# Kernel optimization log

Measured on AMD Instinct MI355X. Metric: run time of the kernel, lower is better.

## Reference

```python
import jax, jax.numpy as jnp
import numpy as np
import math

NEG_INF = -1e30  # stand-in for float('-inf'); softmax/logsumexp treat it identically


def _fnoise(x):
    # factorized NoisyNet transform f(x) = sign(x) * sqrt(|x|)
    return jnp.sign(x) * jnp.sqrt(jnp.abs(x))


def setup_inputs() -> dict:
    B, T, D, E = 4, 4096, 2048, 16
    key = jax.random.key(0)
    ks = jax.random.split(key, 6)
    sigma_init = 0.4 / math.sqrt(D)  # sigma_zero / sqrt(in_features)
    return {
        "mh_output": jax.random.normal(ks[0], (B, T, D), dtype=jnp.float32),
        "weight": jax.random.normal(ks[1], (E, D), dtype=jnp.float32) * 0.02,
        "sigma_weight": jnp.full((E, D), sigma_init, dtype=jnp.float32),
        "bias": jax.random.normal(ks[2], (E,), dtype=jnp.float32) * 0.02,
        "sigma_bias": jnp.full((E,), sigma_init, dtype=jnp.float32),
        "eps_in": jax.random.normal(ks[3], (D,), dtype=jnp.float32),
        "eps_out": jax.random.normal(ks[4], (E,), dtype=jnp.float32),
    }


def reference(mh_output, weight, sigma_weight, bias, sigma_bias, eps_in, eps_out):
    top_k = 2
    E = weight.shape[0]

    # NoisyFactorizedLinear: W' = W + sigma_W * (f(eps_out) f(eps_in)^T)
    f_in = _fnoise(eps_in)            # [D]
    f_out = _fnoise(eps_out)          # [E]
    w_noisy = weight + sigma_weight * (f_out[:, None] * f_in[None, :])  # [E, D]
    b_noisy = bias + sigma_bias * f_out                                 # [E]
    logits = jnp.einsum("btd,ed->bte", mh_output, w_noisy) + b_noisy    # [B,T,E]
    # dropout(p=0.125) is identity in eval mode

    top_vals, indices = jax.lax.top_k(logits, top_k)                    # [B,T,k]
    # scatter top-k back into a -inf-filled tensor == mask of selected experts
    keep = jnp.sum(jax.nn.one_hot(indices, E, dtype=jnp.bool_), axis=-2)  # [B,T,E]
    sparse_logits = jnp.where(keep, logits, NEG_INF)

    router_output = jax.nn.softmax(sparse_logits, axis=-1)

    # z-loss: mean(logsumexp(sparse_logits, -1)^2); only top-k entries survive
    lse = jax.scipy.special.logsumexp(top_vals, axis=-1)                # [B,T]
    z_loss = jnp.mean(lse ** 2)

    return router_output, indices, z_loss
```

## Files before the change

kernel.cpp:

```cpp
#include <hip/hip_runtime.h>
#include <math.h>

#define NROWS 16384
#define DDIM  2048
#define NEXP  16
#define RBLOCKS 512
#define WPB 8

__device__ __forceinline__ float fnoise(float x) {
    return copysignf(sqrtf(fabsf(x)), x);
}


__global__ void prep_kernel(const float* __restrict__ weight,
                            const float* __restrict__ sigma_weight,
                            const float* __restrict__ bias,
                            const float* __restrict__ sigma_bias,
                            const float* __restrict__ eps_in,
                            const float* __restrict__ eps_out,
                            float* __restrict__ w_noisy,
                            float* __restrict__ b_noisy) {
    int idx = blockIdx.x * blockDim.x + threadIdx.x;
    int e = idx >> 11;
    int d = idx & (DDIM - 1);
    float fi = fnoise(eps_in[d]);
    float fo = fnoise(eps_out[e]);
    w_noisy[idx] = weight[idx] + sigma_weight[idx] * fo * fi;
    if (idx < NEXP) {
        b_noisy[idx] = bias[idx] + sigma_bias[idx] * fnoise(eps_out[idx]);
    }
}

__global__ __launch_bounds__(512, 4) void router_kernel(
        const float* __restrict__ x,
        const float* __restrict__ w_noisy,
        const float* __restrict__ b_noisy,
        float* __restrict__ out_router,
        float* __restrict__ out_idx,
        float* __restrict__ zpart) {
    __shared__ float4 wlds[NEXP * 256];

    const int tid  = threadIdx.x;
    const int wv   = tid >> 6;
    const int lane = tid & 63;

    const int rowBase = blockIdx.x * 32 + wv * 4;
    const float4* xr0 = (const float4*)(x + (size_t)(rowBase + 0) * DDIM);
    const float4* xr1 = (const float4*)(x + (size_t)(rowBase + 1) * DDIM);
    const float4* xr2 = (const float4*)(x + (size_t)(rowBase + 2) * DDIM);
    const float4* xr3 = (const float4*)(x + (size_t)(rowBase + 3) * DDIM);

    float acc[64];
    #pragma unroll
    for (int i = 0; i < 64; ++i) acc[i] = 0.0f;

    const float4* wsrc = (const float4*)w_noisy;

    for (int c = 0; c < 2; ++c) {
        if (c) __syncthreads();
        #pragma unroll
        for (int j = 0; j < 8; ++j) {
            int f = j * 512 + tid;
            wlds[f] = wsrc[(f >> 8) * 512 + c * 256 + (f & 255)];
        }
        __syncthreads();

        #pragma unroll 2
        for (int k = 0; k < 4; ++k) {
            int p  = c * 256 + k * 64 + lane;
            int dd = k * 64 + lane;
            float4 xv0 = xr0[p];
            float4 xv1 = xr1[p];
            float4 xv2 = xr2[p];
            float4 xv3 = xr3[p];
            #pragma unroll
            for (int e = 0; e < 16; ++e) {
                float4 w = wlds[e * 256 + dd];
                float s0 = acc[0 * 16 + e];
                float s1 = acc[1 * 16 + e];
                float s2 = acc[2 * 16 + e];
                float s3 = acc[3 * 16 + e];
                s0 = fmaf(xv0.x, w.x, s0); s0 = fmaf(xv0.y, w.y, s0);
                s0 = fmaf(xv0.z, w.z, s0); s0 = fmaf(xv0.w, w.w, s0);
                s1 = fmaf(xv1.x, w.x, s1); s1 = fmaf(xv1.y, w.y, s1);
                s1 = fmaf(xv1.z, w.z, s1); s1 = fmaf(xv1.w, w.w, s1);
                s2 = fmaf(xv2.x, w.x, s2); s2 = fmaf(xv2.y, w.y, s2);
                s2 = fmaf(xv2.z, w.z, s2); s2 = fmaf(xv2.w, w.w, s2);
                s3 = fmaf(xv3.x, w.x, s3); s3 = fmaf(xv3.y, w.y, s3);
                s3 = fmaf(xv3.z, w.z, s3); s3 = fmaf(xv3.w, w.w, s3);
                acc[0 * 16 + e] = s0;
                acc[1 * 16 + e] = s1;
                acc[2 * 16 + e] = s2;
                acc[3 * 16 + e] = s3;
            }
        }
    }

    #pragma unroll
    for (int half = 32; half >= 1; half >>= 1) {
        #pragma unroll
        for (int i = 0; i < half; ++i) {
            bool hi = (lane & half) != 0;
            float keep = hi ? acc[i + half] : acc[i];
            float send = hi ? acc[i] : acc[i + half];
            float recv = __shfl_xor(send, half, 64);
            acc[i] = keep + recv;
        }
    }

    const int e = lane & 15;
    const int r = lane >> 4;
    const int row = rowBase + r;
    float logit = acc[0] + b_noisy[e];

    float m1 = logit; int i1 = e;
    #pragma unroll
    for (int off = 8; off >= 1; off >>= 1) {
        float om = __shfl_xor(m1, off, 64);
        int   oi = __shfl_xor(i1, off, 64);
        if (om > m1 || (om == m1 && oi < i1)) { m1 = om; i1 = oi; }
    }
    float v2 = (e == i1) ? -3.4e38f : logit;
    float m2 = v2; int i2 = e;
    #pragma unroll
    for (int off = 8; off >= 1; off >>= 1) {
        float om = __shfl_xor(m2, off, 64);
        int   oi = __shfl_xor(i2, off, 64);
        if (om > m2 || (om == m2 && oi < i2)) { m2 = om; i2 = oi; }
    }

    float t = expf(m2 - m1);
    float p1 = 1.0f / (1.0f + t);
    float val = (e == i1) ? p1 : ((e == i2) ? t * p1 : 0.0f);
    out_router[(size_t)rowBase * NEXP + lane] = val;

    if (e < 2) {
        out_idx[(size_t)row * 2 + e] = (float)((e == 0) ? i1 : i2);
    }

    float zv = 0.0f;
    if (e == 0) {
        float lse = m1 + log1pf(t);
        zv = lse * lse;
    }
    zv += __shfl_xor(zv, 16, 64);
    zv += __shfl_xor(zv, 32, 64);
    if (lane == 0) {
        zpart[blockIdx.x * WPB + wv] = zv;
    }
}

__global__ void finalize_kernel(const float* __restrict__ zpart,
                                float* __restrict__ out) {
    __shared__ float ws4[4];
    int tid = threadIdx.x;
    float s = 0.0f;
    for (int i = tid; i < RBLOCKS * WPB; i += 256) s += zpart[i];
    #pragma unroll
    for (int off = 32; off >= 1; off >>= 1) s += __shfl_xor(s, off, 64);
    if ((tid & 63) == 0) ws4[tid >> 6] = s;
    __syncthreads();
    if (tid == 0) {
        float total = ws4[0] + ws4[1] + ws4[2] + ws4[3];
        out[NROWS * NEXP + NROWS * 2] = total * (1.0f / (float)NROWS);
    }
}

extern "C" void kernel_launch(void* const* d_in, const int* in_sizes, int n_in,
                              void* d_out, int out_size, void* d_ws, size_t ws_size,
                              hipStream_t stream) {
    const float* mh      = (const float*)d_in[0];
    const float* weight  = (const float*)d_in[1];
    const float* sigw    = (const float*)d_in[2];
    const float* bias    = (const float*)d_in[3];
    const float* sigb    = (const float*)d_in[4];
    const float* eps_in  = (const float*)d_in[5];
    const float* eps_out = (const float*)d_in[6];

    float* out      = (float*)d_out;
    float* w_noisy  = (float*)d_ws;
    float* b_noisy  = w_noisy + NEXP * DDIM;
    float* zpart    = w_noisy + 32800;

    prep_kernel<<<(NEXP * DDIM) / 256, 256, 0, stream>>>(
        weight, sigw, bias, sigb, eps_in, eps_out, w_noisy, b_noisy);

    router_kernel<<<RBLOCKS, 512, 0, stream>>>(
        mh, w_noisy, b_noisy, out, out + NROWS * NEXP, zpart);

    finalize_kernel<<<1, 256, 0, stream>>>(zpart, out);
}
```

Baseline: 215.5 us.

## Double-buffer weight chunks in LDS and prefetch x in smaller blocks

The router kernel now uses 256-thread blocks covering 16 rows, with twice as many blocks. It streams the noisy weight matrix through two 16 KB LDS buffers in 64-float4 chunks, and prefetches the next chunk of x rows and weights into registers while the current chunk is computed. This hides global load latency behind the FMAs and should raise occupancy through the smaller LDS footprint. The cost is extra registers for the prefetch buffers and more barriers and total weight reloads across the larger grid.

```diff
diff --git a/kernel.cpp b/kernel.cpp
--- a/kernel.cpp
+++ b/kernel.cpp
@@ -4,8 +4,9 @@
 #define NROWS 16384
 #define DDIM  2048
 #define NEXP  16
-#define RBLOCKS 512
-#define WPB 8
+#define RBLOCKS 1024
+#define WPB 4
+#define ZN (RBLOCKS * WPB)
 
 __device__ __forceinline__ float fnoise(float x) {
     return copysignf(sqrtf(fabsf(x)), x);
@@ -31,70 +32,89 @@
     }
 }
 
-__global__ __launch_bounds__(512, 4) void router_kernel(
+__global__ __launch_bounds__(256, 4) void router_kernel(
         const float* __restrict__ x,
         const float* __restrict__ w_noisy,
         const float* __restrict__ b_noisy,
         float* __restrict__ out_router,
         float* __restrict__ out_idx,
         float* __restrict__ zpart) {
-    __shared__ float4 wlds[NEXP * 256];
+    __shared__ float4 wlds[2][NEXP * 64];
 
     const int tid  = threadIdx.x;
     const int wv   = tid >> 6;
     const int lane = tid & 63;
 
-    const int rowBase = blockIdx.x * 32 + wv * 4;
+    const int rowBase = blockIdx.x * 16 + wv * 4;
     const float4* xr0 = (const float4*)(x + (size_t)(rowBase + 0) * DDIM);
     const float4* xr1 = (const float4*)(x + (size_t)(rowBase + 1) * DDIM);
     const float4* xr2 = (const float4*)(x + (size_t)(rowBase + 2) * DDIM);
     const float4* xr3 = (const float4*)(x + (size_t)(rowBase + 3) * DDIM);
+    const float4* wsrc = (const float4*)w_noisy;
 
     float acc[64];
     #pragma unroll
     for (int i = 0; i < 64; ++i) acc[i] = 0.0f;
 
-    const float4* wsrc = (const float4*)w_noisy;
-
-    for (int c = 0; c < 2; ++c) {
-        if (c) __syncthreads();
+    float4 xA[4], xB[4], wt[4];
+
+    xA[0] = xr0[lane]; xA[1] = xr1[lane]; xA[2] = xr2[lane]; xA[3] = xr3[lane];
+    #pragma unroll
+    for (int j = 0; j < 4; ++j) {
+        int f = j * 256 + tid;
+        wt[j] = wsrc[(f >> 6) * 512 + (f & 63)];
+    }
+    #pragma unroll
+    for (int j = 0; j < 4; ++j) wlds[0][j * 256 + tid] = wt[j];
+    __syncthreads();
+
+    auto chunk_step = [&](int c, float4 (&xc)[4], float4 (&xn)[4],
+                          const float4* __restrict__ wcur,
+                          float4* __restrict__ wnxt) {
+        if (c < 7) {
+            int p = (c + 1) * 64 + lane;
+            xn[0] = xr0[p]; xn[1] = xr1[p]; xn[2] = xr2[p]; xn[3] = xr3[p];
+            #pragma unroll
+            for (int j = 0; j < 4; ++j) {
+                int f = j * 256 + tid;
+                wt[j] = wsrc[(f >> 6) * 512 + (c + 1) * 64 + (f & 63)];
+            }
+        }
         #pragma unroll
-        for (int j = 0; j < 8; ++j) {
-            int f = j * 512 + tid;
-            wlds[f] = wsrc[(f >> 8) * 512 + c * 256 + (f & 255)];
-        }
-        __syncthreads();
-
-        #pragma unroll 2
-        for (int k = 0; k < 4; ++k) {
-            int p  = c * 256 + k * 64 + lane;
-            int dd = k * 64 + lane;
-            float4 xv0 = xr0[p];
-            float4 xv1 = xr1[p];
-            float4 xv2 = xr2[p];
-            float4 xv3 = xr3[p];
+        for (int e = 0; e < 16; ++e) {
+            float4 w = wcur[e * 64 + lane];
+            float s0 = acc[0 * 16 + e];
+            float s1 = acc[1 * 16 + e];
+            float s2 = acc[2 * 16 + e];
+            float s3 = acc[3 * 16 + e];
+            s0 = fmaf(xc[0].x, w.x, s0); s0 = fmaf(xc[0].y, w.y, s0);
+            s0 = fmaf(xc[0].z, w.z, s0); s0 = fmaf(xc[0].w, w.w, s0);
+            s1 = fmaf(xc[1].x, w.x, s1); s1 = fmaf(xc[1].y, w.y, s1);
+            s1 = fmaf(xc[1].z, w.z, s1); s1 = fmaf(xc[1].w, w.w, s1);
+            s2 = fmaf(xc[2].x, w.x, s2); s2 = fmaf(xc[2].y, w.y, s2);
+            s2 = fmaf(xc[2].z, w.z, s2); s2 = fmaf(xc[2].w, w.w, s2);
+            s3 = fmaf(xc[3].x, w.x, s3); s3 = fmaf(xc[3].y, w.y, s3);
+            s3 = fmaf(xc[3].z, w.z, s3); s3 = fmaf(xc[3].w, w.w, s3);
+            acc[0 * 16 + e] = s0;
+            acc[1 * 16 + e] = s1;
+            acc[2 * 16 + e] = s2;
+            acc[3 * 16 + e] = s3;
+        }
+        if (c < 7) {
             #pragma unroll
-            for (int e = 0; e < 16; ++e) {
-                float4 w = wlds[e * 256 + dd];
-                float s0 = acc[0 * 16 + e];
-                float s1 = acc[1 * 16 + e];
-                float s2 = acc[2 * 16 + e];
-                float s3 = acc[3 * 16 + e];
-                s0 = fmaf(xv0.x, w.x, s0); s0 = fmaf(xv0.y, w.y, s0);
-                s0 = fmaf(xv0.z, w.z, s0); s0 = fmaf(xv0.w, w.w, s0);
-                s1 = fmaf(xv1.x, w.x, s1); s1 = fmaf(xv1.y, w.y, s1);
-                s1 = fmaf(xv1.z, w.z, s1); s1 = fmaf(xv1.w, w.w, s1);
-                s2 = fmaf(xv2.x, w.x, s2); s2 = fmaf(xv2.y, w.y, s2);
-                s2 = fmaf(xv2.z, w.z, s2); s2 = fmaf(xv2.w, w.w, s2);
-                s3 = fmaf(xv3.x, w.x, s3); s3 = fmaf(xv3.y, w.y, s3);
-                s3 = fmaf(xv3.z, w.z, s3); s3 = fmaf(xv3.w, w.w, s3);
-                acc[0 * 16 + e] = s0;
-                acc[1 * 16 + e] = s1;
-                acc[2 * 16 + e] = s2;
-                acc[3 * 16 + e] = s3;
-            }
-        }
-    }
+            for (int j = 0; j < 4; ++j) wnxt[j * 256 + tid] = wt[j];
+            __syncthreads();
+        }
+    };
+
+    chunk_step(0, xA, xB, wlds[0], wlds[1]);
+    chunk_step(1, xB, xA, wlds[1], wlds[0]);
+    chunk_step(2, xA, xB, wlds[0], wlds[1]);
+    chunk_step(3, xB, xA, wlds[1], wlds[0]);
+    chunk_step(4, xA, xB, wlds[0], wlds[1]);
+    chunk_step(5, xB, xA, wlds[1], wlds[0]);
+    chunk_step(6, xA, xB, wlds[0], wlds[1]);
+    chunk_step(7, xB, xA, wlds[1], wlds[0]);
 
     #pragma unroll
     for (int half = 32; half >= 1; half >>= 1) {
@@ -155,7 +175,7 @@
     __shared__ float ws4[4];
     int tid = threadIdx.x;
     float s = 0.0f;
-    for (int i = tid; i < RBLOCKS * WPB; i += 256) s += zpart[i];
+    for (int i = tid; i < ZN; i += 256) s += zpart[i];
     #pragma unroll
     for (int off = 32; off >= 1; off >>= 1) s += __shfl_xor(s, off, 64);
     if ((tid & 63) == 0) ws4[tid >> 6] = s;
@@ -185,7 +205,7 @@
     prep_kernel<<<(NEXP * DDIM) / 256, 256, 0, stream>>>(
         weight, sigw, bias, sigb, eps_in, eps_out, w_noisy, b_noisy);
 
-    router_kernel<<<RBLOCKS, 512, 0, stream>>>(
+    router_kernel<<<RBLOCKS, 256, 0, stream>>>(
         mh, w_noisy, b_noisy, out, out + NROWS * NEXP, zpart);
 
     finalize_kernel<<<1, 256, 0, stream>>>(zpart, out);
```

New measurement: 228.2 us. +5.9%, slower.
